# Optimization experiments

Measured on AMD Instinct MI355X. Metric: run time of the kernel, lower is better.

## Reference

```python
import jax, jax.numpy as jnp
import numpy as np

B, T, D, R = 16, 4096, 512, 256

# Buffers (match torch: linspace(0,T-1,R).long() truncates toward zero)
_LANDMARKS = np.linspace(0.0, T - 1, R).astype(np.int64)
_POS = np.arange(T)[:, None]                                   # [T,1]
_MASK = (_LANDMARKS[None, :] < _POS)                           # [T,R] bool: landmark j < position i
_TDIST = np.clip((_POS.astype(np.float32) - _LANDMARKS[None, :].astype(np.float32)) / T, 0.0, None).astype(np.float32)  # [T,R]


def setup_inputs() -> dict:
    key = jax.random.key(0)
    k1, k2, k3 = jax.random.split(key, 3)
    return {
        "z": jax.random.normal(k1, (B, T, D), dtype=jnp.float32),
        "gegenbauer_weights": jax.random.normal(k2, (3,), dtype=jnp.float32),
        "temporal_alpha": jax.random.normal(k3, (1,), dtype=jnp.float32),
    }


def reference(z, gegenbauer_weights, temporal_alpha):
    dtype = z.dtype
    mask = jnp.asarray(_MASK)                       # [T,R]
    tdist = jnp.asarray(_TDIST, dtype=dtype)        # [T,R]
    lm = jnp.asarray(_LANDMARKS)                    # [R]

    # F.normalize(z, dim=-1) with eps=1e-12
    norm = jnp.linalg.norm(z, axis=-1, keepdims=True)
    Q = z / jnp.maximum(norm, 1e-12)                # [B,T,D]
    K = Q[:, lm, :]                                 # [B,R,D]
    C = jnp.einsum('btd,brd->btr', Q, K)            # [B,T,R] cosine similarity

    # Gegenbauer mixture
    alpha = jax.nn.softmax(gegenbauer_weights)
    C2 = C * C
    P1 = (1.0 + C) * 0.5
    P2 = (3.0 * C2 - 1.0) * 0.5
    P3 = (5.0 * C2 * C - 3.0 * C) * 0.5
    Phi = alpha[0] * P1 + alpha[1] * P2 + alpha[2] * P3

    # Causal mask
    Phi = Phi * mask.astype(dtype)[None, :, :]

    # Temporal decay
    a_td = jax.nn.softplus(temporal_alpha[0])
    Phi = Phi * jnp.exp(-a_td * tdist)[None, :, :]

    # Row-sum normalization
    row_sum = jnp.maximum(Phi.sum(axis=-1, keepdims=True), 1e-6)
    Phi = Phi / row_sum

    # Append constant-ones feature -> [B,T,R+1]
    ones = jnp.ones((Phi.shape[0], Phi.shape[1], 1), dtype=dtype)
    return jnp.concatenate([Phi, ones], axis=-1)
```

## Files before the change

kernel.cpp:

```cpp
#include <hip/hip_runtime.h>
#include <hip/hip_bf16.h>
#include <math.h>

#define B_DIM 16
#define T_DIM 4096
#define D_DIM 512
#define R_DIM 256

#define TM 64
#define BK 64
#define LDP 72
#define NKS (D_DIM/32)

typedef __bf16 bf16x8 __attribute__((ext_vector_type(8)));
typedef float floatx4 __attribute__((ext_vector_type(4)));

__device__ __forceinline__ int landmark_of(int r) {
    if (r >= 255) return 4095;
    const double step = 4095.0 / 255.0;
    return (int)((double)r * step);
}

__device__ __forceinline__ void split_bf16(float x, __bf16& h, __bf16& l) {
    h = (__bf16)x;
    l = (__bf16)(x - (float)h);
}

__global__ void nystrom_prep_kernel(const float* __restrict__ z,
                                    __bf16* __restrict__ Khi, __bf16* __restrict__ Klo) {
    int blk = blockIdx.x;
    int b = blk >> 8;
    int r = blk & 255;
    int lane = threadIdx.x;
    int lm = landmark_of(r);
    const float* src = z + ((size_t)b * T_DIM + lm) * D_DIM + lane * 8;
    float4 v0 = ((const float4*)src)[0];
    float4 v1 = ((const float4*)src)[1];
    float ss = v0.x*v0.x + v0.y*v0.y + v0.z*v0.z + v0.w*v0.w
             + v1.x*v1.x + v1.y*v1.y + v1.z*v1.z + v1.w*v1.w;
    #pragma unroll
    for (int off = 1; off < 64; off <<= 1) ss += __shfl_xor(ss, off, 64);
    float inv = 1.0f / fmaxf(sqrtf(ss), 1e-12f);
    float q[8] = {v0.x*inv, v0.y*inv, v0.z*inv, v0.w*inv,
                  v1.x*inv, v1.y*inv, v1.z*inv, v1.w*inv};
    bf16x8 oh, ol;
    #pragma unroll
    for (int j = 0; j < 8; j++) { __bf16 h, l; split_bf16(q[j], h, l); oh[j] = h; ol[j] = l; }
    size_t dst = ((((size_t)b * NKS + (lane >> 2)) * 16 + (r >> 4)) * 64
                  + (size_t)(lane & 3) * 16 + (r & 15)) * 8;
    *(bf16x8*)(Khi + dst) = oh;
    *(bf16x8*)(Klo + dst) = ol;
}

template<int NACT>
__device__ __forceinline__ void mfma_phase(const __bf16* __restrict__ Ash,
                                           const __bf16* __restrict__ Asl,
                                           const __bf16* __restrict__ khp,
                                           const __bf16* __restrict__ klp,
                                           int koff, int ln, floatx4 (&acc)[4][4]) {
    bf16x8 bh[NACT], bl[NACT];
    #pragma unroll
    for (int ni = 0; ni < NACT; ni++) {
        bh[ni] = *(const bf16x8*)(khp + ni * 2048);
        bl[ni] = *(const bf16x8*)(klp + ni * 2048);
    }
    __builtin_amdgcn_s_setprio(1);
    #pragma unroll
    for (int mi = 0; mi < 4; mi++) {
        bf16x8 afh = *(const bf16x8*)&Ash[(mi * 16 + ln) * LDP + koff];
        bf16x8 afl = *(const bf16x8*)&Asl[(mi * 16 + ln) * LDP + koff];
        #pragma unroll
        for (int ni = 0; ni < NACT; ni++) {
            acc[mi][ni] = __builtin_amdgcn_mfma_f32_16x16x32_bf16(afh, bh[ni], acc[mi][ni], 0, 0, 0);
            acc[mi][ni] = __builtin_amdgcn_mfma_f32_16x16x32_bf16(afh, bl[ni], acc[mi][ni], 0, 0, 0);
            acc[mi][ni] = __builtin_amdgcn_mfma_f32_16x16x32_bf16(afl, bh[ni], acc[mi][ni], 0, 0, 0);
        }
    }
    __builtin_amdgcn_s_setprio(0);
}

__global__ __launch_bounds__(256, 3)
void nystrom_main_kernel(const float* __restrict__ z,
                         const __bf16* __restrict__ Khi, const __bf16* __restrict__ Klo,
                         const float* __restrict__ gw, const float* __restrict__ ta,
                         float* __restrict__ out) {
    __shared__ __attribute__((aligned(16))) char smem[36864];
    __shared__ int   lmtab[R_DIM];
    __shared__ float elmtab[R_DIM];

    float* red    = (float*)(smem);
    float* rnormp = (float*)(smem + 1024);
    float* rinvp  = (float*)(smem + 1280);
    float* rspart = (float*)(smem + 1536);

    const int tid  = threadIdx.x;
    const int b    = blockIdx.y;
    const int t0   = blockIdx.x * TM;
    const int lane = tid & 63;
    const int wv   = tid >> 6;
    const int quad = lane >> 4;
    const int ln   = lane & 15;

    float g0 = gw[0], g1 = gw[1], g2 = gw[2];
    float gm = fmaxf(g0, fmaxf(g1, g2));
    float e0 = expf(g0 - gm), e1 = expf(g1 - gm), e2 = expf(g2 - gm);
    float esum = e0 + e1 + e2;
    float al0 = e0 / esum, al1 = e1 / esum, al2 = e2 / esum;
    float ax = ta[0];
    float a_td = (ax > 20.f) ? ax : log1pf(expf(ax));

    {
        int lm = landmark_of(tid);
        lmtab[tid] = lm;
        elmtab[tid] = expf(a_td * (float)lm * (1.0f / 4096.0f));
    }

    int nact = 0;
    #pragma unroll
    for (int ni = 0; ni < 4; ni++)
        if (landmark_of(ni * 64 + wv * 16) < t0 + TM - 1) nact = ni + 1;

    const int srowA = tid >> 2;
    const int scolA = (tid & 3) * 16;
    const float* zrow = z + ((size_t)b * T_DIM + (t0 + srowA)) * D_DIM + scolA;

    const size_t kfoff = (size_t)b * (NKS * 16 * 64 * 8)
                       + (size_t)wv * 512 + (size_t)lane * 8;
    const __bf16* khb = Khi + kfoff;
    const __bf16* klb = Klo + kfoff;

    floatx4 acc[4][4];
    #pragma unroll
    for (int i = 0; i < 4; i++)
        #pragma unroll
        for (int j = 0; j < 4; j++) acc[i][j] = (floatx4){0.f, 0.f, 0.f, 0.f};
    float ssq = 0.0f;

    float4 a0, a1, a2, a3;

    {
        const float4* ap = (const float4*)(zrow);
        a0 = ap[0]; a1 = ap[1]; a2 = ap[2]; a3 = ap[3];
        float av[16] = {a0.x,a0.y,a0.z,a0.w, a1.x,a1.y,a1.z,a1.w,
                        a2.x,a2.y,a2.z,a2.w, a3.x,a3.y,a3.z,a3.w};
        #pragma unroll
        for (int j = 0; j < 16; j++) ssq += av[j] * av[j];
        __bf16* wsh = (__bf16*)(smem);
        __bf16* wsl = (__bf16*)(smem + 9216);
        #pragma unroll
        for (int g = 0; g < 2; g++) {
            bf16x8 ph, pl;
            #pragma unroll
            for (int j = 0; j < 8; j++) {
                __bf16 h, l; split_bf16(av[g*8+j], h, l); ph[j] = h; pl[j] = l;
            }
            *(bf16x8*)&wsh[srowA * LDP + scolA + g*8] = ph;
            *(bf16x8*)&wsl[srowA * LDP + scolA + g*8] = pl;
        }
    }
    __syncthreads();

    #pragma unroll 1
    for (int kt = 0; kt < D_DIM; kt += BK) {
        const int cur = (kt >> 6) & 1;
        const bool has_next = (kt + BK < D_DIM);

        if (has_next) {
            const float4* ap = (const float4*)(zrow + kt + BK);
            a0 = ap[0]; a1 = ap[1]; a2 = ap[2]; a3 = ap[3];
        }

        const __bf16* Ash = (const __bf16*)(smem + cur * 18432);
        const __bf16* Asl = (const __bf16*)(smem + cur * 18432 + 9216);
        const int ksb = kt >> 5;
        #pragma unroll
        for (int s = 0; s < 2; s++) {
            const __bf16* khp = khb + (size_t)(ksb + s) * 8192;
            const __bf16* klp = klb + (size_t)(ksb + s) * 8192;
            const int koff = s * 32 + quad * 8;
            switch (nact) {
                case 4: mfma_phase<4>(Ash, Asl, khp, klp, koff, ln, acc); break;
                case 3: mfma_phase<3>(Ash, Asl, khp, klp, koff, ln, acc); break;
                case 2: mfma_phase<2>(Ash, Asl, khp, klp, koff, ln, acc); break;
                case 1: mfma_phase<1>(Ash, Asl, khp, klp, koff, ln, acc); break;
                default: break;
            }
        }

        if (has_next) {
            float av[16] = {a0.x,a0.y,a0.z,a0.w, a1.x,a1.y,a1.z,a1.w,
                            a2.x,a2.y,a2.z,a2.w, a3.x,a3.y,a3.z,a3.w};
            #pragma unroll
            for (int j = 0; j < 16; j++) ssq += av[j] * av[j];
            __bf16* wsh = (__bf16*)(smem + (cur ^ 1) * 18432);
            __bf16* wsl = (__bf16*)(smem + (cur ^ 1) * 18432 + 9216);
            #pragma unroll
            for (int g = 0; g < 2; g++) {
                bf16x8 ph, pl;
                #pragma unroll
                for (int j = 0; j < 8; j++) {
                    __bf16 h, l; split_bf16(av[g*8+j], h, l); ph[j] = h; pl[j] = l;
                }
                *(bf16x8*)&wsh[srowA * LDP + scolA + g*8] = ph;
                *(bf16x8*)&wsl[srowA * LDP + scolA + g*8] = pl;
            }
        }
        __syncthreads();
    }

    red[tid] = ssq;
    __syncthreads();
    if (tid < TM) {
        float s = red[tid * 4] + red[tid * 4 + 1] + red[tid * 4 + 2] + red[tid * 4 + 3];
        rnormp[tid] = 1.0f / fmaxf(sqrtf(s), 1e-12f);
    }
    __syncthreads();

    int   lm_r[4];
    float elm_r[4];
    #pragma unroll
    for (int ni = 0; ni < 4; ni++) {
        int r = ni * 64 + wv * 16 + ln;
        lm_r[ni]  = lmtab[r];
        elm_r[ni] = elmtab[r];
    }

    #pragma unroll
    for (int mi = 0; mi < 4; mi++) {
        #pragma unroll
        for (int reg = 0; reg < 4; reg++) {
            int row = mi * 16 + quad * 4 + reg;
            int t = t0 + row;
            float rn = rnormp[row];
            float e_t = __expf(-a_td * (float)t * (1.0f / 4096.0f));
            float s = 0.f;
            #pragma unroll
            for (int ni = 0; ni < 4; ni++) {
                float phi = 0.f;
                if (lm_r[ni] < t) {
                    float c  = acc[mi][ni][reg] * rn;
                    float c2 = c * c;
                    float P1 = 0.5f * (1.f + c);
                    float P2 = 0.5f * (3.f * c2 - 1.f);
                    float P3 = 0.5f * (5.f * c2 * c - 3.f * c);
                    float p  = al0 * P1 + al1 * P2 + al2 * P3;
                    phi = p * e_t * elm_r[ni];
                }
                acc[mi][ni][reg] = phi;
                s += phi;
            }
            #pragma unroll
            for (int off = 1; off < 16; off <<= 1) s += __shfl_xor(s, off, 64);
            if (ln == 0) rspart[wv * TM + row] = s;
        }
    }
    __syncthreads();
    if (tid < TM) {
        float rs = rspart[0 * TM + tid] + rspart[1 * TM + tid]
                 + rspart[2 * TM + tid] + rspart[3 * TM + tid];
        rinvp[tid] = 1.0f / fmaxf(rs, 1e-6f);
    }
    __syncthreads();

    float* ob = out + ((size_t)b * T_DIM + t0) * 257;
    #pragma unroll
    for (int mi = 0; mi < 4; mi++) {
        #pragma unroll
        for (int reg = 0; reg < 4; reg++) {
            int row = mi * 16 + quad * 4 + reg;
            float inv = rinvp[row];
            #pragma unroll
            for (int ni = 0; ni < 4; ni++) {
                int r = ni * 64 + wv * 16 + ln;
                ob[(size_t)row * 257 + r] = acc[mi][ni][reg] * inv;
            }
        }
    }
    if (tid < TM) ob[(size_t)tid * 257 + 256] = 1.0f;
}

extern "C" void kernel_launch(void* const* d_in, const int* in_sizes, int n_in,
                              void* d_out, int out_size, void* d_ws, size_t ws_size,
                              hipStream_t stream) {
    const float* z  = (const float*)d_in[0];
    const float* gw = (const float*)d_in[1];
    const float* ta = (const float*)d_in[2];
    float* out = (float*)d_out;
    __bf16* Khi = (__bf16*)d_ws;
    __bf16* Klo = (__bf16*)((char*)d_ws + (size_t)B_DIM * R_DIM * D_DIM * 2);

    nystrom_prep_kernel<<<dim3(B_DIM * R_DIM), 64, 0, stream>>>(z, Khi, Klo);
    nystrom_main_kernel<<<dim3(T_DIM / TM, B_DIM), 256, 0, stream>>>(z, Khi, Klo, gw, ta, out);
}
```

Baseline: 262.2 us.

## Use 512-thread blocks with 8 waves splitting landmark columns, batch-fastest block order

Doubles the block to 8 waves, so each wave computes 4x2 instead of 4x4 MFMA tiles over the landmark dimension, and each thread loads half as much of z per k-step. Block indices are flattened with the batch index varying fastest, which interleaves batches so consecutive blocks share the same causal workload. The aim is to cut per-wave register pressure and raise the number of waves available to hide latency. The cost is more waves contending for the same LDS tile and more partial sums in the row-norm and row-sum reductions.

```diff
diff --git a/kernel.cpp b/kernel.cpp
--- a/kernel.cpp
+++ b/kernel.cpp
@@ -11,6 +11,7 @@
 #define BK 64
 #define LDP 72
 #define NKS (D_DIM/32)
+#define THREADS 512
 
 typedef __bf16 bf16x8 __attribute__((ext_vector_type(8)));
 typedef float floatx4 __attribute__((ext_vector_type(4)));
@@ -57,12 +58,12 @@
                                            const __bf16* __restrict__ Asl,
                                            const __bf16* __restrict__ khp,
                                            const __bf16* __restrict__ klp,
-                                           int koff, int ln, floatx4 (&acc)[4][4]) {
+                                           int koff, int ln, floatx4 (&acc)[4][2]) {
     bf16x8 bh[NACT], bl[NACT];
     #pragma unroll
     for (int ni = 0; ni < NACT; ni++) {
-        bh[ni] = *(const bf16x8*)(khp + ni * 2048);
-        bl[ni] = *(const bf16x8*)(klp + ni * 2048);
+        bh[ni] = *(const bf16x8*)(khp + ni * 4096);
+        bl[ni] = *(const bf16x8*)(klp + ni * 4096);
     }
     __builtin_amdgcn_s_setprio(1);
     #pragma unroll
@@ -79,7 +80,7 @@
     __builtin_amdgcn_s_setprio(0);
 }
 
-__global__ __launch_bounds__(256, 3)
+__global__ __launch_bounds__(THREADS, 4)
 void nystrom_main_kernel(const float* __restrict__ z,
                          const __bf16* __restrict__ Khi, const __bf16* __restrict__ Klo,
                          const float* __restrict__ gw, const float* __restrict__ ta,
@@ -89,13 +90,14 @@
     __shared__ float elmtab[R_DIM];
 
     float* red    = (float*)(smem);
-    float* rnormp = (float*)(smem + 1024);
-    float* rinvp  = (float*)(smem + 1280);
-    float* rspart = (float*)(smem + 1536);
+    float* rnormp = (float*)(smem + 2048);
+    float* rinvp  = (float*)(smem + 2304);
+    float* rspart = (float*)(smem + 2560);
 
     const int tid  = threadIdx.x;
-    const int b    = blockIdx.y;
-    const int t0   = blockIdx.x * TM;
+    const int bid  = blockIdx.x;
+    const int b    = bid & 15;
+    const int t0   = (bid >> 4) * TM;
     const int lane = tid & 63;
     const int wv   = tid >> 6;
     const int quad = lane >> 4;
@@ -109,7 +111,7 @@
     float ax = ta[0];
     float a_td = (ax > 20.f) ? ax : log1pf(expf(ax));
 
-    {
+    if (tid < R_DIM) {
         int lm = landmark_of(tid);
         lmtab[tid] = lm;
         elmtab[tid] = expf(a_td * (float)lm * (1.0f / 4096.0f));
@@ -117,11 +119,11 @@
 
     int nact = 0;
     #pragma unroll
-    for (int ni = 0; ni < 4; ni++)
-        if (landmark_of(ni * 64 + wv * 16) < t0 + TM - 1) nact = ni + 1;
-
-    const int srowA = tid >> 2;
-    const int scolA = (tid & 3) * 16;
+    for (int ni = 0; ni < 2; ni++)
+        if (landmark_of(ni * 128 + wv * 16) < t0 + TM - 1) nact = ni + 1;
+
+    const int srowA = tid >> 3;
+    const int scolA = (tid & 7) * 8;
     const float* zrow = z + ((size_t)b * T_DIM + (t0 + srowA)) * D_DIM + scolA;
 
     const size_t kfoff = (size_t)b * (NKS * 16 * 64 * 8)
@@ -129,34 +131,26 @@
     const __bf16* khb = Khi + kfoff;
     const __bf16* klb = Klo + kfoff;
 
-    floatx4 acc[4][4];
+    floatx4 acc[4][2];
     #pragma unroll
     for (int i = 0; i < 4; i++)
         #pragma unroll
-        for (int j = 0; j < 4; j++) acc[i][j] = (floatx4){0.f, 0.f, 0.f, 0.f};
+        for (int j = 0; j < 2; j++) acc[i][j] = (floatx4){0.f, 0.f, 0.f, 0.f};
     float ssq = 0.0f;
 
-    float4 a0, a1, a2, a3;
+    float4 a0, a1;
 
     {
         const float4* ap = (const float4*)(zrow);
-        a0 = ap[0]; a1 = ap[1]; a2 = ap[2]; a3 = ap[3];
-        float av[16] = {a0.x,a0.y,a0.z,a0.w, a1.x,a1.y,a1.z,a1.w,
-                        a2.x,a2.y,a2.z,a2.w, a3.x,a3.y,a3.z,a3.w};
-        #pragma unroll
-        for (int j = 0; j < 16; j++) ssq += av[j] * av[j];
-        __bf16* wsh = (__bf16*)(smem);
-        __bf16* wsl = (__bf16*)(smem + 9216);
-        #pragma unroll
-        for (int g = 0; g < 2; g++) {
-            bf16x8 ph, pl;
-            #pragma unroll
-            for (int j = 0; j < 8; j++) {
-                __bf16 h, l; split_bf16(av[g*8+j], h, l); ph[j] = h; pl[j] = l;
-            }
-            *(bf16x8*)&wsh[srowA * LDP + scolA + g*8] = ph;
-            *(bf16x8*)&wsl[srowA * LDP + scolA + g*8] = pl;
-        }
+        a0 = ap[0]; a1 = ap[1];
+        float av[8] = {a0.x,a0.y,a0.z,a0.w, a1.x,a1.y,a1.z,a1.w};
+        #pragma unroll
+        for (int j = 0; j < 8; j++) ssq += av[j] * av[j];
+        bf16x8 ph, pl;
+        #pragma unroll
+        for (int j = 0; j < 8; j++) { __bf16 h, l; split_bf16(av[j], h, l); ph[j] = h; pl[j] = l; }
+        *(bf16x8*)&((__bf16*)(smem))[srowA * LDP + scolA] = ph;
+        *(bf16x8*)&((__bf16*)(smem + 9216))[srowA * LDP + scolA] = pl;
     }
     __syncthreads();
 
@@ -167,7 +161,7 @@
 
         if (has_next) {
             const float4* ap = (const float4*)(zrow + kt + BK);
-            a0 = ap[0]; a1 = ap[1]; a2 = ap[2]; a3 = ap[3];
+            a0 = ap[0]; a1 = ap[1];
         }
 
         const __bf16* Ash = (const __bf16*)(smem + cur * 18432);
@@ -179,8 +173,6 @@
             const __bf16* klp = klb + (size_t)(ksb + s) * 8192;
             const int koff = s * 32 + quad * 8;
             switch (nact) {
-                case 4: mfma_phase<4>(Ash, Asl, khp, klp, koff, ln, acc); break;
-                case 3: mfma_phase<3>(Ash, Asl, khp, klp, koff, ln, acc); break;
                 case 2: mfma_phase<2>(Ash, Asl, khp, klp, koff, ln, acc); break;
                 case 1: mfma_phase<1>(Ash, Asl, khp, klp, koff, ln, acc); break;
                 default: break;
@@ -188,22 +180,14 @@
         }
 
         if (has_next) {
-            float av[16] = {a0.x,a0.y,a0.z,a0.w, a1.x,a1.y,a1.z,a1.w,
-                            a2.x,a2.y,a2.z,a2.w, a3.x,a3.y,a3.z,a3.w};
-            #pragma unroll
-            for (int j = 0; j < 16; j++) ssq += av[j] * av[j];
-            __bf16* wsh = (__bf16*)(smem + (cur ^ 1) * 18432);
-            __bf16* wsl = (__bf16*)(smem + (cur ^ 1) * 18432 + 9216);
-            #pragma unroll
-            for (int g = 0; g < 2; g++) {
-                bf16x8 ph, pl;
-                #pragma unroll
-                for (int j = 0; j < 8; j++) {
-                    __bf16 h, l; split_bf16(av[g*8+j], h, l); ph[j] = h; pl[j] = l;
-                }
-                *(bf16x8*)&wsh[srowA * LDP + scolA + g*8] = ph;
-                *(bf16x8*)&wsl[srowA * LDP + scolA + g*8] = pl;
-            }
+            float av[8] = {a0.x,a0.y,a0.z,a0.w, a1.x,a1.y,a1.z,a1.w};
+            #pragma unroll
+            for (int j = 0; j < 8; j++) ssq += av[j] * av[j];
+            bf16x8 ph, pl;
+            #pragma unroll
+            for (int j = 0; j < 8; j++) { __bf16 h, l; split_bf16(av[j], h, l); ph[j] = h; pl[j] = l; }
+            *(bf16x8*)&((__bf16*)(smem + (cur ^ 1) * 18432))[srowA * LDP + scolA] = ph;
+            *(bf16x8*)&((__bf16*)(smem + (cur ^ 1) * 18432 + 9216))[srowA * LDP + scolA] = pl;
         }
         __syncthreads();
     }
@@ -211,16 +195,18 @@
     red[tid] = ssq;
     __syncthreads();
     if (tid < TM) {
-        float s = red[tid * 4] + red[tid * 4 + 1] + red[tid * 4 + 2] + red[tid * 4 + 3];
+        float s = 0.f;
+        #pragma unroll
+        for (int j = 0; j < 8; j++) s += red[tid * 8 + j];
         rnormp[tid] = 1.0f / fmaxf(sqrtf(s), 1e-12f);
     }
     __syncthreads();
 
-    int   lm_r[4];
-    float elm_r[4];
-    #pragma unroll
-    for (int ni = 0; ni < 4; ni++) {
-        int r = ni * 64 + wv * 16 + ln;
+    int   lm_r[2];
+    float elm_r[2];
+    #pragma unroll
+    for (int ni = 0; ni < 2; ni++) {
+        int r = ni * 128 + wv * 16 + ln;
         lm_r[ni]  = lmtab[r];
         elm_r[ni] = elmtab[r];
     }
@@ -235,7 +221,7 @@
             float e_t = __expf(-a_td * (float)t * (1.0f / 4096.0f));
             float s = 0.f;
             #pragma unroll
-            for (int ni = 0; ni < 4; ni++) {
+            for (int ni = 0; ni < 2; ni++) {
                 float phi = 0.f;
                 if (lm_r[ni] < t) {
                     float c  = acc[mi][ni][reg] * rn;
@@ -256,8 +242,9 @@
     }
     __syncthreads();
     if (tid < TM) {
-        float rs = rspart[0 * TM + tid] + rspart[1 * TM + tid]
-                 + rspart[2 * TM + tid] + rspart[3 * TM + tid];
+        float rs = 0.f;
+        #pragma unroll
+        for (int w = 0; w < 8; w++) rs += rspart[w * TM + tid];
         rinvp[tid] = 1.0f / fmaxf(rs, 1e-6f);
     }
     __syncthreads();
@@ -270,8 +257,8 @@
             int row = mi * 16 + quad * 4 + reg;
             float inv = rinvp[row];
             #pragma unroll
-            for (int ni = 0; ni < 4; ni++) {
-                int r = ni * 64 + wv * 16 + ln;
+            for (int ni = 0; ni < 2; ni++) {
+                int r = ni * 128 + wv * 16 + ln;
                 ob[(size_t)row * 257 + r] = acc[mi][ni][reg] * inv;
             }
         }
@@ -290,5 +277,5 @@
     __bf16* Klo = (__bf16*)((char*)d_ws + (size_t)B_DIM * R_DIM * D_DIM * 2);
 
     nystrom_prep_kernel<<<dim3(B_DIM * R_DIM), 64, 0, stream>>>(z, Khi, Klo);
-    nystrom_main_kernel<<<dim3(T_DIM / TM, B_DIM), 256, 0, stream>>>(z, Khi, Klo, gw, ta, out);
-}
+    nystrom_main_kernel<<<dim3((T_DIM / TM) * B_DIM), THREADS, 0, stream>>>(z, Khi, Klo, gw, ta, out);
+}
```

Result: no change. 264.5 us (+0.9%).
